# Kernel optimization log

Measured on AMD Instinct MI355X. Metric: run time of the kernel, lower is better.

## Reference

```python
import jax, jax.numpy as jnp
import numpy as np

MIN_SUPPORT = 20.0
MAX_BEAR_ERROR = 20.0
AVG_ERROR = 0.05    # opt.cross_R_and_D_average_error
WEIGHT = 1.0        # opt.cross_weight_R_and_D


def setup_inputs() -> dict:
    key = jax.random.key(0)
    ks = jax.random.split(key, 14)
    bs, N, M, K, D = 16, 2048, 2048, 32, 128
    f32 = jnp.float32
    return {
        "r_tokens_full": jax.random.normal(ks[0], (bs, K, D), f32),
        "r_tokens_partial": jax.random.normal(ks[1], (bs, K, D), f32),
        "pc_seg_partial": jax.random.randint(ks[2], (bs, N, K), 0, 2).astype(f32),
        "pc_seg_full": jax.random.randint(ks[3], (bs, N, K), 0, 2).astype(f32),
        "pc_partial": jax.random.normal(ks[4], (bs, N, 3), f32),
        "deformed": jax.random.normal(ks[5], (bs, 3, M), f32),
        "p_rot": jax.random.normal(ks[6], (bs, 3, 3), f32),
        "p_t": jax.random.normal(ks[7], (bs, 1, 3), f32),
        "f_rot": jax.random.normal(ks[8], (bs, 3, 3), f32),
        "f_t": jax.random.normal(ks[9], (bs, 1, 3), f32),
        "tgt_rand_rot": jax.random.normal(ks[10], (bs, 3, 3), f32),
        "tgt_rand_t": jax.random.normal(ks[11], (bs, 1, 3), f32),
        "src_rand_rot": jax.random.normal(ks[12], (bs, 3, 3), f32),
        "src_rand_t": jax.random.normal(ks[13], (bs, 1, 3), f32),
    }


def reference(r_tokens_full, r_tokens_partial, pc_seg_partial, pc_seg_full,
              pc_partial, deformed, p_rot, p_t, f_rot, f_t,
              tgt_rand_rot, tgt_rand_t, src_rand_rot, src_rand_t):
    # --- get_cons_shape: chain of rigid transforms mapping partial pc into full frame
    z = jnp.matmul(pc_partial, p_rot) + p_t                       # [bs,N,3]
    z = jnp.matmul(z - tgt_rand_t, tgt_rand_rot.transpose(0, 2, 1))
    z = jnp.matmul(z, src_rand_rot) + src_rand_t
    x = jnp.matmul(z - f_t, f_rot.transpose(0, 2, 1))             # pc_partial_at_full [bs,N,3]

    # --- knn_points K=1: squared distance to nearest neighbor in deformed cloud
    y = deformed.transpose(0, 2, 1)                               # [bs,M,3]
    d2 = (jnp.sum(x * x, -1)[:, :, None]
          + jnp.sum(y * y, -1)[:, None, :]
          - 2.0 * jnp.einsum('bnd,bmd->bnm', x, y))               # [bs,N,M]
    cham_x = jnp.maximum(jnp.min(d2, axis=-1), 0.0)               # [bs,N]

    # seg^T @ cham: per-keypoint aggregated chamfer loss
    seg2def = jnp.einsum('bnk,bn->bk', pc_seg_partial, cham_x)    # [bs,K]

    sup_p = jnp.sum(pc_seg_partial, axis=1)                       # [bs,K]
    sup_f = jnp.sum(pc_seg_full, axis=1)                          # [bs,K]
    valid = (sup_p >= MIN_SUPPORT) & (sup_f >= MIN_SUPPORT)

    sp = jnp.maximum(sup_p, 1.0)
    sf = jnp.maximum(sup_f, 1.0)
    rel = jax.nn.sigmoid(seg2def / sp / AVG_ERROR)                # [bs,K]
    r_dis = jnp.sum((r_tokens_full / sf[..., None]
                     - r_tokens_partial / sp[..., None]) ** 2, axis=-1)
    loss_rd = (r_dis - rel) ** 2                                  # [bs,K]

    mask = valid & (loss_rd <= MAX_BEAR_ERROR)
    nofL = jnp.sum(mask).astype(loss_rd.dtype)
    total = jnp.sum(jnp.where(mask, loss_rd, 0.0))
    return total / (nofL + 1.0) * WEIGHT
```

## Files before the change

kernel.cpp:

```cpp
#include <hip/hip_runtime.h>
#include <math.h>

#define BS 16
#define NPTS 2048
#define MPTS 2048
#define KSEG 32
#define DDIM 128

#define OFF_XN    0
#define OFF_PART  32768
#define OFF_SEGP  294912
#define OFF_LOSSP 307200

__global__ __launch_bounds__(256) void cham_kernel(
    const float* __restrict__ pc_partial, const float* __restrict__ deformed,
    const float* __restrict__ p_rot, const float* __restrict__ p_t,
    const float* __restrict__ f_rot, const float* __restrict__ f_t,
    const float* __restrict__ tg_rot, const float* __restrict__ tg_t,
    const float* __restrict__ sr_rot, const float* __restrict__ sr_t,
    float* __restrict__ xnArr, float* __restrict__ part)
{
    __shared__ float4 sh_y[256];
    __shared__ float pmin[4][512];

    const int bid  = blockIdx.x;
    const int b    = bid >> 5;
    const int r    = bid & 31;
    const int tile = r & 3;
    const int sg   = r >> 2;
    const int t = threadIdx.x;
    const int l = t & 63;
    const int w = t >> 6;

    const float* def0 = deformed + (size_t)b * 3 * MPTS + sg * 256;
    {
        float y0 = def0[t], y1 = def0[MPTS + t], y2 = def0[2*MPTS + t];
        sh_y[t] = make_float4(y0, y1, y2, 0.5f*(y0*y0 + y1*y1 + y2*y2));
    }

    float R[9], T[3];
    {
        float P[9], F[9], Tg[9], Sr[9];
#pragma unroll
        for (int i = 0; i < 9; i++) {
            P[i] = p_rot[b*9+i];  F[i] = f_rot[b*9+i];
            Tg[i] = tg_rot[b*9+i]; Sr[i] = sr_rot[b*9+i];
        }
        float A[9], Bm[9];
#pragma unroll
        for (int i = 0; i < 3; i++)
#pragma unroll
            for (int j = 0; j < 3; j++)
                A[i*3+j] = P[i*3+0]*Tg[j*3+0] + P[i*3+1]*Tg[j*3+1] + P[i*3+2]*Tg[j*3+2];
#pragma unroll
        for (int i = 0; i < 3; i++)
#pragma unroll
            for (int j = 0; j < 3; j++)
                Bm[i*3+j] = A[i*3+0]*Sr[0*3+j] + A[i*3+1]*Sr[1*3+j] + A[i*3+2]*Sr[2*3+j];
#pragma unroll
        for (int i = 0; i < 3; i++)
#pragma unroll
            for (int j = 0; j < 3; j++)
                R[i*3+j] = Bm[i*3+0]*F[j*3+0] + Bm[i*3+1]*F[j*3+1] + Bm[i*3+2]*F[j*3+2];
        float t0[3], t1[3], t2[3], t3[3];
#pragma unroll
        for (int i = 0; i < 3; i++) t0[i] = p_t[b*3+i] - tg_t[b*3+i];
#pragma unroll
        for (int j = 0; j < 3; j++)
            t1[j] = t0[0]*Tg[j*3+0] + t0[1]*Tg[j*3+1] + t0[2]*Tg[j*3+2];
#pragma unroll
        for (int j = 0; j < 3; j++)
            t2[j] = t1[0]*Sr[0*3+j] + t1[1]*Sr[1*3+j] + t1[2]*Sr[2*3+j];
#pragma unroll
        for (int i = 0; i < 3; i++) t3[i] = t2[i] + sr_t[b*3+i] - f_t[b*3+i];
#pragma unroll
        for (int j = 0; j < 3; j++)
            T[j] = t3[0]*F[j*3+0] + t3[1]*F[j*3+1] + t3[2]*F[j*3+2];
    }

    float x0[8], x1[8], x2[8], mn[8];
    const int nbase = tile * 512 + l;
    const float* pcb = pc_partial + (size_t)b * NPTS * 3;
#pragma unroll
    for (int j = 0; j < 8; j++) {
        const float* pc = pcb + (size_t)(nbase + 64*j) * 3;
        float px = pc[0], py = pc[1], pz = pc[2];
        x0[j] = px*R[0] + py*R[3] + pz*R[6] + T[0];
        x1[j] = px*R[1] + py*R[4] + pz*R[7] + T[1];
        x2[j] = px*R[2] + py*R[5] + pz*R[8] + T[2];
        mn[j] = 3.402823466e+38f;
    }
    if (sg == 0 && w == 0) {
#pragma unroll
        for (int j = 0; j < 8; j++)
            xnArr[(size_t)b*NPTS + nbase + 64*j] =
                x0[j]*x0[j] + x1[j]*x1[j] + x2[j]*x2[j];
    }
    __syncthreads();

    const int mb = w * 64;
#pragma unroll 4
    for (int i = 0; i < 64; i++) {
        float4 y = sh_y[mb + i];
#pragma unroll
        for (int j = 0; j < 8; j++) {
            float s = fmaf(-x2[j], y.z, fmaf(-x1[j], y.y, fmaf(-x0[j], y.x, y.w)));
            mn[j] = fminf(mn[j], s);
        }
    }

#pragma unroll
    for (int j = 0; j < 8; j++) pmin[w][64*j + l] = mn[j];
    __syncthreads();

#pragma unroll
    for (int u = 0; u < 2; u++) {
        int p = t + 256 * u;
        float v = fminf(fminf(pmin[0][p], pmin[1][p]),
                        fminf(pmin[2][p], pmin[3][p]));
        part[(size_t)sg * (BS*NPTS) + (size_t)b * NPTS + tile*512 + p] = v;
    }
}

__global__ __launch_bounds__(256) void seg_kernel(
    const float* __restrict__ seg_p, const float* __restrict__ seg_f,
    const float* __restrict__ xnArr, const float* __restrict__ part,
    float* __restrict__ ws)
{
    __shared__ float chamLDS[256];
    __shared__ float red0[1024], red1[1024], red2[1024];

    const int b = blockIdx.x >> 3;
    const int nc = blockIdx.x & 7;
    const int t = threadIdx.x;
    const int n0 = nc * 256;

    {
        const size_t nidx = (size_t)b * NPTS + n0 + t;
        float xn = xnArr[nidx];
        float pm = part[nidx];
#pragma unroll
        for (int sg = 1; sg < 8; sg++)
            pm = fminf(pm, part[(size_t)sg * (BS*NPTS) + nidx]);
        chamLDS[t] = fmaxf(fmaf(2.0f, pm, xn), 0.0f);
    }
    __syncthreads();

    const int l = t & 63;
    const int w = t >> 6;
    const int rowoff = l >> 3;
    const int k4 = l & 7;
    const float4* sp4 = (const float4*)(seg_p + ((size_t)b * NPTS + n0) * KSEG);
    const float4* sf4 = (const float4*)(seg_f + ((size_t)b * NPTS + n0) * KSEG);

    float4 ap = make_float4(0.f,0.f,0.f,0.f);
    float4 af = make_float4(0.f,0.f,0.f,0.f);
    float4 a2 = make_float4(0.f,0.f,0.f,0.f);
#pragma unroll
    for (int i = 0; i < 8; i++) {
        int n = w * 64 + i * 8 + rowoff;
        float c = chamLDS[n];
        float4 vp = sp4[n * 8 + k4];
        float4 vf = sf4[n * 8 + k4];
        ap.x += vp.x; ap.y += vp.y; ap.z += vp.z; ap.w += vp.w;
        af.x += vf.x; af.y += vf.y; af.z += vf.z; af.w += vf.w;
        a2.x = fmaf(vp.x, c, a2.x); a2.y = fmaf(vp.y, c, a2.y);
        a2.z = fmaf(vp.z, c, a2.z); a2.w = fmaf(vp.w, c, a2.w);
    }
    red0[t*4+0] = ap.x; red0[t*4+1] = ap.y; red0[t*4+2] = ap.z; red0[t*4+3] = ap.w;
    red1[t*4+0] = af.x; red1[t*4+1] = af.y; red1[t*4+2] = af.z; red1[t*4+3] = af.w;
    red2[t*4+0] = a2.x; red2[t*4+1] = a2.y; red2[t*4+2] = a2.z; red2[t*4+3] = a2.w;
    __syncthreads();

    if (t < KSEG) {
        float s0 = 0.f, s1 = 0.f, s2 = 0.f;
#pragma unroll
        for (int j = 0; j < 32; j++) {
            s0 += red0[j*32 + t];
            s1 += red1[j*32 + t];
            s2 += red2[j*32 + t];
        }
        ws[OFF_SEGP + ((0*BS + b)*8 + nc)*KSEG + t] = s0;
        ws[OFF_SEGP + ((1*BS + b)*8 + nc)*KSEG + t] = s1;
        ws[OFF_SEGP + ((2*BS + b)*8 + nc)*KSEG + t] = s2;
    }
}

__global__ __launch_bounds__(256) void loss_kernel(
    const float* __restrict__ rf_tok, const float* __restrict__ rp_tok,
    float* __restrict__ ws)
{
    const int b  = blockIdx.x >> 1;
    const int kh = blockIdx.x & 1;
    const int t = threadIdx.x;
    const int cell = t >> 4;
    const int dg   = t & 15;
    const int k = kh * 16 + cell;

    float supp = 0.f, supf = 0.f;
#pragma unroll
    for (int nc = 0; nc < 8; nc++) {
        supp += ws[OFF_SEGP + ((0*BS + b)*8 + nc)*KSEG + k];
        supf += ws[OFF_SEGP + ((1*BS + b)*8 + nc)*KSEG + k];
    }
    const float spv = fmaxf(supp, 1.0f);
    const float sfv = fmaxf(supf, 1.0f);

    const float* rf = rf_tok + ((size_t)b * KSEG + k) * DDIM;
    const float* rp = rp_tok + ((size_t)b * KSEG + k) * DDIM;
    float acc = 0.f;
#pragma unroll
    for (int j = 0; j < 8; j++) {
        int d = dg + 16 * j;
        float v = rf[d] / sfv - rp[d] / spv;
        acc += v * v;
    }
#pragma unroll
    for (int off = 8; off; off >>= 1) acc += __shfl_xor(acc, off);

    __shared__ float lbuf[16], cbuf[16];
    if (dg == 0) {
        float s2d = 0.f;
#pragma unroll
        for (int nc = 0; nc < 8; nc++)
            s2d += ws[OFF_SEGP + ((2*BS + b)*8 + nc)*KSEG + k];
        bool valid = (supp >= 20.0f) && (supf >= 20.0f);
        float arg = s2d / spv / 0.05f;
        float rel = 1.0f / (1.0f + expf(-arg));
        float ld = acc - rel; ld = ld * ld;
        bool msk = valid && (ld <= 20.0f);
        lbuf[cell] = msk ? ld : 0.0f;
        cbuf[cell] = msk ? 1.0f : 0.0f;
    }
    __syncthreads();
    if (t == 0) {
        float st = 0.f, sc = 0.f;
#pragma unroll
        for (int i = 0; i < 16; i++) { st += lbuf[i]; sc += cbuf[i]; }
        ws[OFF_LOSSP + blockIdx.x]      = st;
        ws[OFF_LOSSP + 32 + blockIdx.x] = sc;
    }
}

__global__ __launch_bounds__(64) void final_kernel(
    const float* __restrict__ ws, float* __restrict__ out)
{
    const int t = threadIdx.x;
    float v1 = (t < 32) ? ws[OFF_LOSSP + t] : 0.0f;
    float v2 = (t < 32) ? ws[OFF_LOSSP + 32 + t] : 0.0f;
#pragma unroll
    for (int off = 16; off; off >>= 1) {
        v1 += __shfl_xor(v1, off);
        v2 += __shfl_xor(v2, off);
    }
    if (t == 0) out[0] = v1 / (v2 + 1.0f) * 1.0f;
}

extern "C" void kernel_launch(void* const* d_in, const int* in_sizes, int n_in,
                              void* d_out, int out_size, void* d_ws, size_t ws_size,
                              hipStream_t stream) {
    const float* r_tokens_full    = (const float*)d_in[0];
    const float* r_tokens_partial = (const float*)d_in[1];
    const float* pc_seg_partial   = (const float*)d_in[2];
    const float* pc_seg_full      = (const float*)d_in[3];
    const float* pc_partial       = (const float*)d_in[4];
    const float* deformed         = (const float*)d_in[5];
    const float* p_rot            = (const float*)d_in[6];
    const float* p_t              = (const float*)d_in[7];
    const float* f_rot            = (const float*)d_in[8];
    const float* f_t              = (const float*)d_in[9];
    const float* tgt_rand_rot     = (const float*)d_in[10];
    const float* tgt_rand_t       = (const float*)d_in[11];
    const float* src_rand_rot     = (const float*)d_in[12];
    const float* src_rand_t       = (const float*)d_in[13];

    float* ws  = (float*)d_ws;
    float* out = (float*)d_out;

    cham_kernel<<<BS * 32, 256, 0, stream>>>(
        pc_partial, deformed, p_rot, p_t, f_rot, f_t,
        tgt_rand_rot, tgt_rand_t, src_rand_rot, src_rand_t,
        ws + OFF_XN, ws + OFF_PART);

    seg_kernel<<<BS * 8, 256, 0, stream>>>(
        pc_seg_partial, pc_seg_full, ws + OFF_XN, ws + OFF_PART, ws);

    loss_kernel<<<BS * 2, 256, 0, stream>>>(r_tokens_full, r_tokens_partial, ws);

    final_kernel<<<1, 64, 0, stream>>>(ws, out);
}
```

Baseline: 101.3 us.

## Fuse chamfer and segment reduction kernels; fold final reduction into loss kernel

Merges the nearest-neighbour chamfer kernel with the segment aggregation kernel. Each 512-thread block now holds all 2048 deformed points in LDS and handles 128 query points, so partial minima no longer make a round trip through global memory. The final scalar reduction moves into the loss kernel using a last-block atomic counter, which removes two kernel launches. In exchange the grid shrinks to 256 blocks that each need large LDS, which may lower occupancy. The counter reset in the first kernel relies on stream ordering.

```diff
diff --git a/kernel.cpp b/kernel.cpp
--- a/kernel.cpp
+++ b/kernel.cpp
@@ -7,35 +7,48 @@
 #define KSEG 32
 #define DDIM 128
 
-#define OFF_XN    0
-#define OFF_PART  32768
-#define OFF_SEGP  294912
-#define OFF_LOSSP 307200
-
-__global__ __launch_bounds__(256) void cham_kernel(
+#define NTILE 16
+#define PPB 128
+
+#define OFF_SEGP  0
+#define OFF_LOSSP 24576
+#define OFF_CNT   24640
+
+__global__ __launch_bounds__(512) void cham_seg_kernel(
     const float* __restrict__ pc_partial, const float* __restrict__ deformed,
     const float* __restrict__ p_rot, const float* __restrict__ p_t,
     const float* __restrict__ f_rot, const float* __restrict__ f_t,
     const float* __restrict__ tg_rot, const float* __restrict__ tg_t,
     const float* __restrict__ sr_rot, const float* __restrict__ sr_t,
-    float* __restrict__ xnArr, float* __restrict__ part)
+    const float* __restrict__ seg_p, const float* __restrict__ seg_f,
+    float* __restrict__ ws)
 {
-    __shared__ float4 sh_y[256];
-    __shared__ float pmin[4][512];
+    __shared__ union {
+        float4 y[2048];
+        float  red[3][2048];
+    } sm;
+    __shared__ float pmin[16][PPB];
+    __shared__ float xnLDS[PPB];
+    __shared__ float chamLDS[PPB];
 
     const int bid  = blockIdx.x;
-    const int b    = bid >> 5;
-    const int r    = bid & 31;
-    const int tile = r & 3;
-    const int sg   = r >> 2;
-    const int t = threadIdx.x;
-    const int l = t & 63;
-    const int w = t >> 6;
-
-    const float* def0 = deformed + (size_t)b * 3 * MPTS + sg * 256;
-    {
-        float y0 = def0[t], y1 = def0[MPTS + t], y2 = def0[2*MPTS + t];
-        sh_y[t] = make_float4(y0, y1, y2, 0.5f*(y0*y0 + y1*y1 + y2*y2));
+    const int b    = bid >> 4;
+    const int tile = bid & 15;
+    const int t  = threadIdx.x;
+    const int l  = t & 63;
+    const int w  = t >> 6;
+    const int h  = l >> 5;
+    const int ll = l & 31;
+    const int s  = w * 2 + h;
+
+    if (bid == 0 && t == 0) ((int*)ws)[OFF_CNT] = 0;
+
+    const float* def0 = deformed + (size_t)b * 3 * MPTS;
+#pragma unroll
+    for (int i = 0; i < 4; i++) {
+        int m = i * 512 + t;
+        float y0 = def0[m], y1 = def0[MPTS + m], y2 = def0[2*MPTS + m];
+        sm.y[m] = make_float4(y0, y1, y2, 0.5f*(y0*y0 + y1*y1 + y2*y2));
     }
 
     float R[9], T[3];
@@ -78,87 +91,57 @@
             T[j] = t3[0]*F[j*3+0] + t3[1]*F[j*3+1] + t3[2]*F[j*3+2];
     }
 
-    float x0[8], x1[8], x2[8], mn[8];
-    const int nbase = tile * 512 + l;
+    const int n0 = tile * PPB;
     const float* pcb = pc_partial + (size_t)b * NPTS * 3;
-#pragma unroll
-    for (int j = 0; j < 8; j++) {
-        const float* pc = pcb + (size_t)(nbase + 64*j) * 3;
+    float x0[4], x1[4], x2[4], xn[4], mn[4];
+#pragma unroll
+    for (int j = 0; j < 4; j++) {
+        const float* pc = pcb + (size_t)(n0 + ll + 32*j) * 3;
         float px = pc[0], py = pc[1], pz = pc[2];
         x0[j] = px*R[0] + py*R[3] + pz*R[6] + T[0];
         x1[j] = px*R[1] + py*R[4] + pz*R[7] + T[1];
         x2[j] = px*R[2] + py*R[5] + pz*R[8] + T[2];
+        xn[j] = x0[j]*x0[j] + x1[j]*x1[j] + x2[j]*x2[j];
         mn[j] = 3.402823466e+38f;
     }
-    if (sg == 0 && w == 0) {
-#pragma unroll
-        for (int j = 0; j < 8; j++)
-            xnArr[(size_t)b*NPTS + nbase + 64*j] =
-                x0[j]*x0[j] + x1[j]*x1[j] + x2[j]*x2[j];
-    }
-    __syncthreads();
-
-    const int mb = w * 64;
+    if (t < 32) {
+#pragma unroll
+        for (int j = 0; j < 4; j++) xnLDS[ll + 32*j] = xn[j];
+    }
+    __syncthreads();
+
+    const float4* yb = sm.y + s * 128;
 #pragma unroll 4
-    for (int i = 0; i < 64; i++) {
-        float4 y = sh_y[mb + i];
-#pragma unroll
-        for (int j = 0; j < 8; j++) {
-            float s = fmaf(-x2[j], y.z, fmaf(-x1[j], y.y, fmaf(-x0[j], y.x, y.w)));
-            mn[j] = fminf(mn[j], s);
-        }
-    }
-
-#pragma unroll
-    for (int j = 0; j < 8; j++) pmin[w][64*j + l] = mn[j];
-    __syncthreads();
-
-#pragma unroll
-    for (int u = 0; u < 2; u++) {
-        int p = t + 256 * u;
-        float v = fminf(fminf(pmin[0][p], pmin[1][p]),
-                        fminf(pmin[2][p], pmin[3][p]));
-        part[(size_t)sg * (BS*NPTS) + (size_t)b * NPTS + tile*512 + p] = v;
-    }
-}
-
-__global__ __launch_bounds__(256) void seg_kernel(
-    const float* __restrict__ seg_p, const float* __restrict__ seg_f,
-    const float* __restrict__ xnArr, const float* __restrict__ part,
-    float* __restrict__ ws)
-{
-    __shared__ float chamLDS[256];
-    __shared__ float red0[1024], red1[1024], red2[1024];
-
-    const int b = blockIdx.x >> 3;
-    const int nc = blockIdx.x & 7;
-    const int t = threadIdx.x;
-    const int n0 = nc * 256;
-
-    {
-        const size_t nidx = (size_t)b * NPTS + n0 + t;
-        float xn = xnArr[nidx];
-        float pm = part[nidx];
-#pragma unroll
-        for (int sg = 1; sg < 8; sg++)
-            pm = fminf(pm, part[(size_t)sg * (BS*NPTS) + nidx]);
-        chamLDS[t] = fmaxf(fmaf(2.0f, pm, xn), 0.0f);
-    }
-    __syncthreads();
-
-    const int l = t & 63;
-    const int w = t >> 6;
+    for (int i = 0; i < 128; i++) {
+        float4 y = yb[i];
+#pragma unroll
+        for (int j = 0; j < 4; j++) {
+            float sc = fmaf(-x2[j], y.z, fmaf(-x1[j], y.y, fmaf(-x0[j], y.x, y.w)));
+            mn[j] = fminf(mn[j], sc);
+        }
+    }
+#pragma unroll
+    for (int j = 0; j < 4; j++) pmin[s][ll + 32*j] = mn[j];
+    __syncthreads();
+
+    if (t < PPB) {
+        float v = pmin[0][t];
+#pragma unroll
+        for (int q = 1; q < 16; q++) v = fminf(v, pmin[q][t]);
+        chamLDS[t] = fmaxf(fmaf(2.0f, v, xnLDS[t]), 0.0f);
+    }
+    __syncthreads();
+
     const int rowoff = l >> 3;
     const int k4 = l & 7;
     const float4* sp4 = (const float4*)(seg_p + ((size_t)b * NPTS + n0) * KSEG);
     const float4* sf4 = (const float4*)(seg_f + ((size_t)b * NPTS + n0) * KSEG);
-
     float4 ap = make_float4(0.f,0.f,0.f,0.f);
     float4 af = make_float4(0.f,0.f,0.f,0.f);
     float4 a2 = make_float4(0.f,0.f,0.f,0.f);
 #pragma unroll
-    for (int i = 0; i < 8; i++) {
-        int n = w * 64 + i * 8 + rowoff;
+    for (int i = 0; i < 2; i++) {
+        int n = w * 16 + i * 8 + rowoff;
         float c = chamLDS[n];
         float4 vp = sp4[n * 8 + k4];
         float4 vf = sf4[n * 8 + k4];
@@ -167,28 +150,28 @@
         a2.x = fmaf(vp.x, c, a2.x); a2.y = fmaf(vp.y, c, a2.y);
         a2.z = fmaf(vp.z, c, a2.z); a2.w = fmaf(vp.w, c, a2.w);
     }
-    red0[t*4+0] = ap.x; red0[t*4+1] = ap.y; red0[t*4+2] = ap.z; red0[t*4+3] = ap.w;
-    red1[t*4+0] = af.x; red1[t*4+1] = af.y; red1[t*4+2] = af.z; red1[t*4+3] = af.w;
-    red2[t*4+0] = a2.x; red2[t*4+1] = a2.y; red2[t*4+2] = a2.z; red2[t*4+3] = a2.w;
+    sm.red[0][t*4+0] = ap.x; sm.red[0][t*4+1] = ap.y; sm.red[0][t*4+2] = ap.z; sm.red[0][t*4+3] = ap.w;
+    sm.red[1][t*4+0] = af.x; sm.red[1][t*4+1] = af.y; sm.red[1][t*4+2] = af.z; sm.red[1][t*4+3] = af.w;
+    sm.red[2][t*4+0] = a2.x; sm.red[2][t*4+1] = a2.y; sm.red[2][t*4+2] = a2.z; sm.red[2][t*4+3] = a2.w;
     __syncthreads();
 
     if (t < KSEG) {
         float s0 = 0.f, s1 = 0.f, s2 = 0.f;
 #pragma unroll
-        for (int j = 0; j < 32; j++) {
-            s0 += red0[j*32 + t];
-            s1 += red1[j*32 + t];
-            s2 += red2[j*32 + t];
-        }
-        ws[OFF_SEGP + ((0*BS + b)*8 + nc)*KSEG + t] = s0;
-        ws[OFF_SEGP + ((1*BS + b)*8 + nc)*KSEG + t] = s1;
-        ws[OFF_SEGP + ((2*BS + b)*8 + nc)*KSEG + t] = s2;
+        for (int j = 0; j < 64; j++) {
+            s0 += sm.red[0][j*32 + t];
+            s1 += sm.red[1][j*32 + t];
+            s2 += sm.red[2][j*32 + t];
+        }
+        ws[OFF_SEGP + ((0*BS + b)*NTILE + tile)*KSEG + t] = s0;
+        ws[OFF_SEGP + ((1*BS + b)*NTILE + tile)*KSEG + t] = s1;
+        ws[OFF_SEGP + ((2*BS + b)*NTILE + tile)*KSEG + t] = s2;
     }
 }
 
 __global__ __launch_bounds__(256) void loss_kernel(
     const float* __restrict__ rf_tok, const float* __restrict__ rp_tok,
-    float* __restrict__ ws)
+    float* __restrict__ ws, float* __restrict__ out)
 {
     const int b  = blockIdx.x >> 1;
     const int kh = blockIdx.x & 1;
@@ -199,9 +182,9 @@
 
     float supp = 0.f, supf = 0.f;
 #pragma unroll
-    for (int nc = 0; nc < 8; nc++) {
-        supp += ws[OFF_SEGP + ((0*BS + b)*8 + nc)*KSEG + k];
-        supf += ws[OFF_SEGP + ((1*BS + b)*8 + nc)*KSEG + k];
+    for (int nc = 0; nc < NTILE; nc++) {
+        supp += ws[OFF_SEGP + ((0*BS + b)*NTILE + nc)*KSEG + k];
+        supf += ws[OFF_SEGP + ((1*BS + b)*NTILE + nc)*KSEG + k];
     }
     const float spv = fmaxf(supp, 1.0f);
     const float sfv = fmaxf(supf, 1.0f);
@@ -222,8 +205,8 @@
     if (dg == 0) {
         float s2d = 0.f;
 #pragma unroll
-        for (int nc = 0; nc < 8; nc++)
-            s2d += ws[OFF_SEGP + ((2*BS + b)*8 + nc)*KSEG + k];
+        for (int nc = 0; nc < NTILE; nc++)
+            s2d += ws[OFF_SEGP + ((2*BS + b)*NTILE + nc)*KSEG + k];
         bool valid = (supp >= 20.0f) && (supf >= 20.0f);
         float arg = s2d / spv / 0.05f;
         float rel = 1.0f / (1.0f + expf(-arg));
@@ -233,27 +216,36 @@
         cbuf[cell] = msk ? 1.0f : 0.0f;
     }
     __syncthreads();
+
+    __shared__ int isLast;
     if (t == 0) {
         float st = 0.f, sc = 0.f;
 #pragma unroll
         for (int i = 0; i < 16; i++) { st += lbuf[i]; sc += cbuf[i]; }
         ws[OFF_LOSSP + blockIdx.x]      = st;
         ws[OFF_LOSSP + 32 + blockIdx.x] = sc;
-    }
-}
-
-__global__ __launch_bounds__(64) void final_kernel(
-    const float* __restrict__ ws, float* __restrict__ out)
-{
-    const int t = threadIdx.x;
-    float v1 = (t < 32) ? ws[OFF_LOSSP + t] : 0.0f;
-    float v2 = (t < 32) ? ws[OFF_LOSSP + 32 + t] : 0.0f;
-#pragma unroll
-    for (int off = 16; off; off >>= 1) {
-        v1 += __shfl_xor(v1, off);
-        v2 += __shfl_xor(v2, off);
-    }
-    if (t == 0) out[0] = v1 / (v2 + 1.0f) * 1.0f;
+        __threadfence();
+        int prev = atomicAdd((int*)ws + OFF_CNT, 1);
+        isLast = (prev == 31) ? 1 : 0;
+    }
+    __syncthreads();
+
+    if (isLast) {
+        __threadfence();
+        float v1 = 0.f, v2 = 0.f;
+        if (t < 32) {
+            v1 = __hip_atomic_load(ws + OFF_LOSSP + t,
+                                   __ATOMIC_RELAXED, __HIP_MEMORY_SCOPE_AGENT);
+            v2 = __hip_atomic_load(ws + OFF_LOSSP + 32 + t,
+                                   __ATOMIC_RELAXED, __HIP_MEMORY_SCOPE_AGENT);
+        }
+#pragma unroll
+        for (int off = 16; off; off >>= 1) {
+            v1 += __shfl_xor(v1, off);
+            v2 += __shfl_xor(v2, off);
+        }
+        if (t == 0) out[0] = v1 / (v2 + 1.0f) * 1.0f;
+    }
 }
 
 extern "C" void kernel_launch(void* const* d_in, const int* in_sizes, int n_in,
@@ -277,15 +269,11 @@
     float* ws  = (float*)d_ws;
     float* out = (float*)d_out;
 
-    cham_kernel<<<BS * 32, 256, 0, stream>>>(
+    cham_seg_kernel<<<BS * NTILE, 512, 0, stream>>>(
         pc_partial, deformed, p_rot, p_t, f_rot, f_t,
         tgt_rand_rot, tgt_rand_t, src_rand_rot, src_rand_t,
-        ws + OFF_XN, ws + OFF_PART);
-
-    seg_kernel<<<BS * 8, 256, 0, stream>>>(
-        pc_seg_partial, pc_seg_full, ws + OFF_XN, ws + OFF_PART, ws);
-
-    loss_kernel<<<BS * 2, 256, 0, stream>>>(r_tokens_full, r_tokens_partial, ws);
-
-    final_kernel<<<1, 64, 0, stream>>>(ws, out);
+        pc_seg_partial, pc_seg_full, ws);
+
+    loss_kernel<<<BS * 2, 256, 0, stream>>>(
+        r_tokens_full, r_tokens_partial, ws, out);
 }
```

Result: no change. 102.1 us (+0.8%).
